# Kernel optimization log

Measured on AMD Instinct MI355X. Metric: run time of the kernel, lower is better.

The kernel has to match this reference:

```python
import jax, jax.numpy as jnp
import numpy as np

B, T, OBS, ACT, H, S = 512, 64, 1024, 32, 1024, 64


def setup_inputs() -> dict:
    key = jax.random.key(0)
    ks = jax.random.split(key, 16)
    w = lambda k, shape: 0.02 * jax.random.normal(k, shape, jnp.float32)
    return {
        "obs": jax.random.normal(ks[0], (B, T, OBS), jnp.float32),
        "action": jax.random.normal(ks[1], (B, T, ACT), jnp.float32),
        "eps": jax.random.normal(ks[2], (B, T, S), jnp.float32),
        # obs encoder: Linear(OBS->H) + ReLU
        "W_enc": w(ks[3], (H, OBS)), "b_enc": jnp.zeros((H,), jnp.float32),
        # GRUCell(stoch+action -> H), torch gate order: r, z, n
        "W_ih": w(ks[4], (3 * H, S + ACT)), "W_hh": w(ks[5], (3 * H, H)),
        "b_ih": jnp.zeros((3 * H,), jnp.float32), "b_hh": jnp.zeros((3 * H,), jnp.float32),
        # prior: Linear(H -> 2S); posterior: Linear(2H -> 2S)
        "W_prior": w(ks[6], (2 * S, H)), "b_prior": jnp.zeros((2 * S,), jnp.float32),
        "W_post": w(ks[7], (2 * S, 2 * H)), "b_post": jnp.zeros((2 * S,), jnp.float32),
        # decoder: Linear(H+S -> H) ReLU Linear(H -> OBS)
        "W_dec1": w(ks[8], (H, H + S)), "b_dec1": jnp.zeros((H,), jnp.float32),
        "W_dec2": w(ks[9], (OBS, H)), "b_dec2": jnp.zeros((OBS,), jnp.float32),
        # reward / done heads: Linear(H+S -> 1)
        "W_rew": w(ks[10], (1, H + S)), "b_rew": jnp.zeros((1,), jnp.float32),
        "W_done": w(ks[11], (1, H + S)), "b_done": jnp.zeros((1,), jnp.float32),
    }


def _stats(x):
    mean, raw_std = jnp.split(x, 2, axis=-1)
    return mean, jax.nn.softplus(raw_std) + 1e-4


def reference(obs, action, eps, W_enc, b_enc, W_ih, W_hh, b_ih, b_hh,
              W_prior, b_prior, W_post, b_post, W_dec1, b_dec1, W_dec2, b_dec2,
              W_rew, b_rew, W_done, b_done):
    batch = obs.shape[0]
    hid = W_hh.shape[1]
    sdim = eps.shape[-1]
    # obs encoder is per-step independent -> batch it over time up front
    emb_all = jax.nn.relu(jnp.einsum('bto,ho->bth', obs, W_enc) + b_enc)

    def step(carry, xs):
        deter, stoch = carry
        a_t, emb_t, eps_t = xs
        # torch GRUCell
        x = jnp.concatenate([stoch, a_t], axis=-1)
        gi = x @ W_ih.T + b_ih
        gh = deter @ W_hh.T + b_hh
        i_r, i_z, i_n = jnp.split(gi, 3, axis=-1)
        h_r, h_z, h_n = jnp.split(gh, 3, axis=-1)
        r = jax.nn.sigmoid(i_r + h_r)
        z = jax.nn.sigmoid(i_z + h_z)
        n = jnp.tanh(i_n + r * h_n)
        deter = (1.0 - z) * n + z * deter
        # prior / posterior stats
        p_mean, p_std = _stats(deter @ W_prior.T + b_prior)
        q_mean, q_std = _stats(jnp.concatenate([deter, emb_t], axis=-1) @ W_post.T + b_post)
        stoch = q_mean + eps_t * q_std  # reparam sample
        feat = jnp.concatenate([deter, stoch], axis=-1)
        pred = jax.nn.relu(feat @ W_dec1.T + b_dec1) @ W_dec2.T + b_dec2
        rew = feat @ W_rew.T + b_rew
        done = feat @ W_done.T + b_done
        kl = jnp.log(p_std / q_std) + (q_std ** 2 + (q_mean - p_mean) ** 2) / (2.0 * p_std ** 2) - 0.5
        return (deter, stoch), (pred, rew, done, kl.mean(axis=-1, keepdims=True))

    init = (jnp.zeros((batch, hid), obs.dtype), jnp.zeros((batch, sdim), obs.dtype))
    xs = (jnp.swapaxes(action, 0, 1), jnp.swapaxes(emb_all, 0, 1), jnp.swapaxes(eps, 0, 1))
    _, (preds, rews, dones, kls) = jax.lax.scan(step, init, xs)
    pred = jnp.swapaxes(preds, 0, 1)    # [B,T,OBS]
    reward = jnp.swapaxes(rews, 0, 1)   # [B,T,1]
    done = jnp.swapaxes(dones, 0, 1)    # [B,T,1]
    kl = kls.mean()
    return pred, reward, done, kl
```

## Files before the change

kernel.cpp:

```cpp
#include <hip/hip_runtime.h>
#include <stdint.h>

#define BB 512
#define TT 64
#define OBSD 1024
#define ACTD 32
#define HD 1024
#define SD 64
#define BT (BB*TT)
#define G3 (3*HD)
#define STRD ((long)TT*HD)

typedef unsigned int uint32;
typedef unsigned long long ull;
typedef unsigned short u16;
typedef __attribute__((ext_vector_type(8))) short bf16x8;
typedef __attribute__((ext_vector_type(4))) float f32x4;

__device__ __forceinline__ float bf2f(u16 v){ uint32_t u = ((uint32_t)v)<<16; return __builtin_bit_cast(float,u); }
__device__ __forceinline__ u16 f2bf(float f){ uint32_t u = __builtin_bit_cast(uint32_t,f); uint32_t r = (u + 0x7FFFu + ((u>>16)&1u))>>16; return (u16)r; }
__device__ __forceinline__ float sigm(float x){ return 1.f/(1.f+expf(-x)); }
#define MFMA __builtin_amdgcn_mfma_f32_16x16x32_bf16

__device__ __forceinline__ void gload16(const u16* g, u16* l){
  __builtin_amdgcn_global_load_lds(
      (const __attribute__((address_space(1))) u16*)g,
      (__attribute__((address_space(3))) u16*)l, 16, 0, 0);
}

__global__ void cvt_kernel(const float* __restrict__ in, u16* __restrict__ out, long n){
  long i = (long)blockIdx.x*blockDim.x + threadIdx.x;
  long st = (long)gridDim.x*blockDim.x;
  for (; i<n; i+=st) out[i] = f2bf(in[i]);
}

struct GemmP {
  const u16* a0; const u16* a1; const u16* a2;
  const u16* b0; const u16* b1; const u16* b2;
  long lda0, lda1, lda2, ldb0, ldb1, ldb2;
  int kc0, kc1, kc2, kcPerZ;
  float* cf; u16* cb;
  long ldc, ldcb, zstride;
  const float* bias0; const float* bias1;
  int relu;
};

template<int BM,int BN>
__global__ __launch_bounds__(256) void gemm_bf16(GemmP p){
  __shared__ __align__(16) u16 sAB[2][(BM+BN)*32];
  const int m0 = blockIdx.y*BM, n0 = blockIdx.x*BN;
  const int tid = threadIdx.x, lane = tid&63, wave = tid>>6;
  const int wm = (wave>>1)*(BM/2), wn = (wave&1)*(BN/2);
  constexpr int FM = BM/32, FN = BN/32;
  f32x4 acc[FM][FN] = {};
  const int cbeg = blockIdx.z*p.kcPerZ;
  int cend = cbeg + p.kcPerZ; if (cend > p.kc2) cend = p.kc2;
  const int kg = lane>>4, lr = lane&15;
  const int srow = lane>>2, scol = (lane&3)*8;

  auto STAGE = [&](int buf, int c){
    const u16* ap; const u16* bp; long lda, ldb; int kofs;
    if (c < p.kc0){ ap=p.a0; bp=p.b0; lda=p.lda0; ldb=p.ldb0; kofs=c*32; }
    else if (c < p.kc1){ ap=p.a1; bp=p.b1; lda=p.lda1; ldb=p.ldb1; kofs=(c-p.kc0)*32; }
    else { ap=p.a2; bp=p.b2; lda=p.lda2; ldb=p.ldb2; kofs=(c-p.kc1)*32; }
    u16* base = sAB[buf];
    #pragma unroll
    for (int it=0; it<BM/64; ++it){
      int row = it*64 + wave*16 + srow;
      gload16(ap + (long)(m0+row)*lda + kofs + scol,
              base + (it*64 + wave*16)*32);
    }
    #pragma unroll
    for (int it=0; it<BN/64; ++it){
      int row = it*64 + wave*16 + srow;
      gload16(bp + (long)(n0+row)*ldb + kofs + scol,
              base + BM*32 + (it*64 + wave*16)*32);
    }
  };

  STAGE(0, cbeg);
  for (int c=cbeg;c<cend;++c){
    const int cur = (c-cbeg)&1;
    asm volatile("s_waitcnt vmcnt(0)" ::: "memory");
    __syncthreads();
    if (c+1 < cend) STAGE(cur^1, c+1);
    const u16* sA = sAB[cur];
    const u16* sB = sAB[cur] + BM*32;
    bf16x8 af[FM], bfv[FN];
    #pragma unroll
    for (int i=0;i<FM;++i) af[i] = *(const bf16x8*)&sA[(wm+i*16+lr)*32 + kg*8];
    #pragma unroll
    for (int j=0;j<FN;++j) bfv[j] = *(const bf16x8*)&sB[(wn+j*16+lr)*32 + kg*8];
    #pragma unroll
    for (int i=0;i<FM;++i)
      #pragma unroll
      for (int j=0;j<FN;++j)
        acc[i][j] = MFMA(af[i], bfv[j], acc[i][j], 0,0,0);
    __syncthreads();
  }
  const bool partial = (gridDim.z > 1);
  float* cf = p.cf ? (p.cf + (partial ? (long)blockIdx.z*p.zstride : 0)) : nullptr;
  #pragma unroll
  for (int i=0;i<FM;++i){
    #pragma unroll
    for (int j=0;j<FN;++j){
      const int gr0 = m0 + wm + i*16 + kg*4;
      const int gc = n0 + wn + j*16 + lr;
      float bias = 0.f;
      if (!partial){
        if (p.bias0) bias += p.bias0[gc];
        if (p.bias1) bias += p.bias1[gc];
      }
      #pragma unroll
      for (int r=0;r<4;++r){
        float v = acc[i][j][r] + bias;
        if (p.relu) v = fmaxf(v, 0.f);
        const long row = gr0 + r;
        if (cf) cf[row*p.ldc + gc] = v;
        if (p.cb) p.cb[row*p.ldcb + gc] = f2bf(v);
      }
    }
  }
}

struct ScanArgs {
  const u16* act; const u16* Wih; const u16* Whh;
  const float* b_ih; const float* b_hh;
  const u16* Wpos; const float* qemb; const float* eps;
  u16* det; u16* sto; float* qm; float* qs;
  uint32* slots;
};

__device__ __forceinline__ void gsync_g(uint32* slots, int m, int n, uint32 val){
  asm volatile("s_waitcnt vmcnt(0)" ::: "memory");
  __syncthreads();
  if (threadIdx.x == 0)
    __hip_atomic_store(&slots[m*64 + n], val, __ATOMIC_RELAXED, __HIP_MEMORY_SCOPE_AGENT);
  if (threadIdx.x < 32){
    while (__hip_atomic_load(&slots[m*64 + threadIdx.x], __ATOMIC_RELAXED,
                             __HIP_MEMORY_SCOPE_AGENT) < val)
      __builtin_amdgcn_s_sleep(2);
  }
  __syncthreads();
}

#define SA2 152

__global__ __launch_bounds__(256, 1) void scan_kernel(ScanArgs A){
  __shared__ __align__(16) u16 lds[(64+96)*SA2];
  u16* sA = lds; u16* sB = lds + 64*SA2;
  float* pf = (float*)lds;
  const int bid = blockIdx.x;
  const int tid = threadIdx.x, lane = tid&63, wave = tid>>6;
  const int lr = lane&15, kg = lane>>4;
  const int n = bid&31, m = bid>>5;
  const int m0 = m*64, h0 = n*32;
  const int wrow = (wave&1)*32, wcol = (wave>>1)*16;

  const int srow = tid>>4;
  const int scu  = (tid&15)*8;

  long whhb[6], wihb[6];
  #pragma unroll
  for (int i=0;i<6;++i){
    int br = srow + i*16;
    int gate = br>>5, hr = br&31;
    whhb[i] = (long)(gate*HD + h0 + hr)*HD + scu;
    wihb[i] = (long)(gate*HD + h0 + hr)*96 + scu;
  }

  const int h4 = h0 + wcol + kg*4;
  float bir[4], bhr[4], biz[4], bhz[4], bin[4], bhn[4];
  #pragma unroll
  for (int r=0;r<4;++r){
    bir[r]=A.b_ih[h4+r];      bhr[r]=A.b_hh[h4+r];
    biz[r]=A.b_ih[HD+h4+r];   bhz[r]=A.b_hh[HD+h4+r];
    bin[r]=A.b_ih[2*HD+h4+r]; bhn[r]=A.b_hh[2*HD+h4+r];
  }

  const int pj = n & 3, prt = n >> 2;

  float dreg[2][4] = {{0.f,0.f,0.f,0.f},{0.f,0.f,0.f,0.f}};
  const bf16x8 zerov = {};

  bf16x8 pa[4], pb[6];
  auto loadgt = [&](int tt, int g){
    if (g < 8){
      if (tt > 0){
        const u16* s = A.det + (long)(tt-1)*HD + g*128 + scu;
        #pragma unroll
        for (int j=0;j<4;++j) pa[j] = *(const bf16x8*)(s + (long)(m0+srow+16*j)*STRD);
      } else { pa[0]=zerov; pa[1]=zerov; pa[2]=zerov; pa[3]=zerov; }
      #pragma unroll
      for (int i=0;i<6;++i) pb[i] = *(const bf16x8*)(A.Whh + whhb[i] + g*128);
    } else {
      if (scu < 64){
        if (tt > 0){
          #pragma unroll
          for (int j=0;j<4;++j)
            pa[j] = *(const bf16x8*)(A.sto + (long)(m0+srow+16*j)*((long)TT*SD) + (long)(tt-1)*SD + scu);
        } else { pa[0]=zerov; pa[1]=zerov; pa[2]=zerov; pa[3]=zerov; }
      } else if (scu < 96){
        #pragma unroll
        for (int j=0;j<4;++j)
          pa[j] = *(const bf16x8*)(A.act + (long)(m0+srow+16*j)*((long)TT*ACTD) + (long)tt*ACTD + (scu-64));
      } else { pa[0]=zerov; pa[1]=zerov; pa[2]=zerov; pa[3]=zerov; }
      #pragma unroll
      for (int i=0;i<6;++i) pb[i] = (scu < 96) ? *(const bf16x8*)(A.Wih + wihb[i]) : zerov;
    }
  };

  loadgt(0, 0);
  for (int t=0; t<TT; ++t){
    f32x4 aR[2]={}, aZ[2]={}, aNd[2]={}, aNx[2]={};
    for (int g=0; g<9; ++g){
      __syncthreads();
      #pragma unroll
      for (int j=0;j<4;++j) *(bf16x8*)&sA[(srow+16*j)*SA2 + scu] = pa[j];
      #pragma unroll
      for (int i=0;i<6;++i) *(bf16x8*)&sB[(srow+16*i)*SA2 + scu] = pb[i];
      if (g < 8) loadgt(t, g+1);
      __syncthreads();
      #pragma unroll
      for (int k=0;k<4;++k){
        bf16x8 a0v = *(const bf16x8*)&sA[(wrow+lr)*SA2 + k*32 + kg*8];
        bf16x8 a1v = *(const bf16x8*)&sA[(wrow+16+lr)*SA2 + k*32 + kg*8];
        bf16x8 b0 = *(const bf16x8*)&sB[(wcol+lr)*SA2 + k*32 + kg*8];
        bf16x8 b1 = *(const bf16x8*)&sB[(32+wcol+lr)*SA2 + k*32 + kg*8];
        bf16x8 b2 = *(const bf16x8*)&sB[(64+wcol+lr)*SA2 + k*32 + kg*8];
        aR[0] = MFMA(b0,a0v,aR[0],0,0,0); aR[1] = MFMA(b0,a1v,aR[1],0,0,0);
        aZ[0] = MFMA(b1,a0v,aZ[0],0,0,0); aZ[1] = MFMA(b1,a1v,aZ[1],0,0,0);
        if (g<8){ aNd[0] = MFMA(b2,a0v,aNd[0],0,0,0); aNd[1] = MFMA(b2,a1v,aNd[1],0,0,0); }
        else    { aNx[0] = MFMA(b2,a0v,aNx[0],0,0,0); aNx[1] = MFMA(b2,a1v,aNx[1],0,0,0); }
      }
    }
    #pragma unroll
    for (int rf=0;rf<2;++rf){
      const long brow = m0 + wrow + rf*16 + lr;
      u16 pk[4];
      #pragma unroll
      for (int r=0;r<4;++r){
        float rr = sigm(aR[rf][r]+bir[r]+bhr[r]);
        float z  = sigm(aZ[rf][r]+biz[r]+bhz[r]);
        float nn = tanhf(aNx[rf][r]+bin[r] + rr*(aNd[rf][r]+bhn[r]));
        float d = (1.f - z)*nn + z*dreg[rf][r];
        dreg[rf][r] = d;
        pk[r] = f2bf(d);
      }
      ull pv; __builtin_memcpy(&pv, pk, 8);
      __hip_atomic_store((ull*)(A.det + brow*STRD + (long)t*HD + h4), pv,
                         __ATOMIC_RELAXED, __HIP_MEMORY_SCOPE_AGENT);
    }
    gsync_g(A.slots, m, n, (uint32)(2*t+1));
    {
      f32x4 accM = {}, accS = {};
      const int k0 = wave*256;
      const u16* arow = A.det + (long)(m0 + prt*8 + (lr&7))*STRD + (long)t*HD + k0 + kg*8;
      const u16* bm = A.Wpos + (long)(pj*16 + lr)*(2*HD) + k0 + kg*8;
      const u16* bs = A.Wpos + (long)(64 + pj*16 + lr)*(2*HD) + k0 + kg*8;
      #pragma unroll
      for (int kk=0; kk<8; ++kk){
        bf16x8 af = *(const bf16x8*)(arow + kk*32);
        accM = MFMA(af, *(const bf16x8*)(bm + kk*32), accM, 0,0,0);
        accS = MFMA(af, *(const bf16x8*)(bs + kk*32), accS, 0,0,0);
      }
      #pragma unroll
      for (int r=0;r<4;++r){
        int rowt = kg*4 + r;
        pf[wave*512 + rowt*16 + lr]       = accM[r];
        pf[wave*512 + 256 + rowt*16 + lr] = accS[r];
      }
      __syncthreads();
      if (tid < 64){
        const int row = tid>>3;
        const int s2 = (tid&7)*2;
        const long grow = m0 + prt*8 + row;
        const float* qe = A.qemb + grow*((long)TT*128) + (long)t*128;
        const float* ep = A.eps  + grow*((long)TT*SD) + (long)t*SD;
        u16 spk[2];
        #pragma unroll
        for (int i=0;i<2;++i){
          int sl = s2 + i, sg = pj*16 + sl;
          float mean = pf[row*16+sl] + pf[512+row*16+sl] + pf[1024+row*16+sl] + pf[1536+row*16+sl];
          float rsv  = pf[256+row*16+sl] + pf[768+row*16+sl] + pf[1280+row*16+sl] + pf[1792+row*16+sl];
          mean += qe[sg];
          rsv  += qe[64+sg];
          float sp = fmaxf(rsv,0.f) + log1pf(expf(-fabsf(rsv)));
          float qs_ = sp + 1e-4f;
          float st = mean + ep[sg]*qs_;
          A.qm[grow*((long)TT*SD) + (long)t*SD + sg] = mean;
          A.qs[grow*((long)TT*SD) + (long)t*SD + sg] = qs_;
          spk[i] = f2bf(st);
        }
        uint32 pv; __builtin_memcpy(&pv, spk, 4);
        __hip_atomic_store((uint32*)(A.sto + grow*((long)TT*SD) + (long)t*SD + pj*16 + s2), pv,
                           __ATOMIC_RELAXED, __HIP_MEMORY_SCOPE_AGENT);
      }
      __syncthreads();
    }
    if (t+1 < TT) loadgt(t+1, 0);
    gsync_g(A.slots, m, n, (uint32)(2*t+2));
  }
}

__global__ __launch_bounds__(256) void gru_step(
    const u16* __restrict__ sto_prev, long ssto,
    const u16* __restrict__ act_t,
    const u16* __restrict__ det_prev, long sdet,
    const u16* __restrict__ Wih, const u16* __restrict__ Whh,
    const float* __restrict__ b_ih, const float* __restrict__ b_hh,
    float* __restrict__ deterF, u16* __restrict__ det_bf_t){
  constexpr int SA = 40;
  __shared__ u16 sA[32*SA];
  __shared__ u16 sB[96*SA];
  const int id = blockIdx.x;
  const int n = (id&7) + ((id>>7)<<3);
  const int m = (id>>3)&15;
  const int m0 = m*32, h0 = n*32;
  const int tid = threadIdx.x, lane = tid&63, wave = tid>>6;
  const int wm = wave>>1, wn = wave&1;
  const int lr = lane&15, kg = lane>>4;

  f32x4 aR = {}, aZ = {}, aNd = {}, aNx = {};

  auto aAddr = [&](int c, int row, int sc)->const u16*{
    if (c < 32) return det_prev + (long)(m0+row)*sdet + c*32 + sc;
    if (c < 34) return sto_prev + (long)(m0+row)*ssto + (c-32)*32 + sc;
    return act_t + (long)(m0+row)*((long)TT*ACTD) + sc;
  };
  auto bAddr = [&](int c, int l)->const u16*{
    int row = l>>2, sc = (l&3)*8;
    int g = row>>5, hr = row&31;
    if (c < 32) return Whh + (long)(g*1024 + h0 + hr)*HD + c*32 + sc;
    return Wih + (long)(g*1024 + h0 + hr)*(SD+ACTD) + (c-32)*32 + sc;
  };

  bf16x8 rA, rB0, rB1;
  auto loadc = [&](int c){
    rB0 = *(const bf16x8*)bAddr(c, tid);
    if (tid < 128){
      rA  = *(const bf16x8*)aAddr(c, tid>>2, (tid&3)*8);
      rB1 = *(const bf16x8*)bAddr(c, 256+tid);
    }
  };

  loadc(0);
  for (int c=0; c<35; ++c){
    *(bf16x8*)&sB[(tid>>2)*SA + (tid&3)*8] = rB0;
    if (tid < 128){
      *(bf16x8*)&sA[(tid>>2)*SA + (tid&3)*8] = rA;
      int l = 256+tid;
      *(bf16x8*)&sB[(l>>2)*SA + (l&3)*8] = rB1;
    }
    if (c < 34) loadc(c+1);
    __syncthreads();
    bf16x8 af = *(const bf16x8*)&sA[(wm*16+lr)*SA + kg*8];
    bf16x8 b0 = *(const bf16x8*)&sB[(     wn*16+lr)*SA + kg*8];
    bf16x8 b1 = *(const bf16x8*)&sB[(32 + wn*16+lr)*SA + kg*8];
    bf16x8 b2 = *(const bf16x8*)&sB[(64 + wn*16+lr)*SA + kg*8];
    aR = MFMA(af,b0,aR,0,0,0);
    aZ = MFMA(af,b1,aZ,0,0,0);
    if (c < 32) aNd = MFMA(af,b2,aNd,0,0,0);
    else        aNx = MFMA(af,b2,aNx,0,0,0);
    __syncthreads();
  }

  const int col = h0 + wn*16 + lr;
  const float bir = b_ih[col],      bhr = b_hh[col];
  const float biz = b_ih[col+HD],   bhz = b_hh[col+HD];
  const float bin = b_ih[col+2*HD], bhn = b_hh[col+2*HD];
  #pragma unroll
  for (int reg=0; reg<4; ++reg){
    const int row = m0 + wm*16 + kg*4 + reg;
    float r = sigm(aR[reg] + bir + bhr);
    float z = sigm(aZ[reg] + biz + bhz);
    float nn = tanhf(aNx[reg] + bin + r*(aNd[reg] + bhn));
    const long fidx = (long)row*HD + col;
    float d = (1.f - z)*nn + z*deterF[fidx];
    deterF[fidx] = d;
    det_bf_t[(long)row*STRD + col] = f2bf(d);
  }
}

__global__ __launch_bounds__(256) void post_step(
    const u16* __restrict__ det_t,
    const u16* __restrict__ Wpos,
    const float* __restrict__ qemb_t,
    const float* __restrict__ eps_t,
    float* __restrict__ qm_t, float* __restrict__ qs_t, u16* __restrict__ sto_out){
  constexpr int SA = 40;
  __shared__ u16 sA4[4*16*SA];
  __shared__ u16 sB4[4*128*SA];
  const int m0 = blockIdx.x*16;
  const int tid = threadIdx.x, lane = tid&63, w = tid>>6;
  const int lr = lane&15, kg = lane>>4;

  f32x4 acc[8] = {};
  bf16x8 rA, rB[8];
  auto loadIter = [&](int i){
    #pragma unroll
    for (int rnd=0; rnd<8; ++rnd){
      int l = rnd*256 + tid;
      int q = l>>9, row = (l>>2)&127, sc = (l&3)*8;
      rB[rnd] = *(const bf16x8*)(Wpos + (long)row*(2*HD) + (q*8+i)*32 + sc);
    }
    { int q = tid>>6, row = (tid>>2)&15, sc = (tid&3)*8;
      rA = *(const bf16x8*)(det_t + (long)(m0+row)*STRD + (q*8+i)*32 + sc); }
  };

  loadIter(0);
  for (int i=0; i<8; ++i){
    #pragma unroll
    for (int rnd=0; rnd<8; ++rnd){
      int l = rnd*256 + tid;
      int q = l>>9, row = (l>>2)&127, sc = (l&3)*8;
      *(bf16x8*)&sB4[q*128*SA + row*SA + sc] = rB[rnd];
    }
    { int q = tid>>6, row = (tid>>2)&15, sc = (tid&3)*8;
      *(bf16x8*)&sA4[q*16*SA + row*SA + sc] = rA; }
    if (i < 7) loadIter(i+1);
    __syncthreads();
    bf16x8 af = *(const bf16x8*)&sA4[w*16*SA + lr*SA + kg*8];
    #pragma unroll
    for (int j=0; j<8; ++j){
      bf16x8 bf = *(const bf16x8*)&sB4[w*128*SA + (j*16+lr)*SA + kg*8];
      acc[j] = MFMA(af, bf, acc[j], 0,0,0);
    }
    __syncthreads();
  }

  float* pf = (float*)sB4;
  #pragma unroll
  for (int j=0; j<8; ++j)
    #pragma unroll
    for (int reg=0; reg<4; ++reg)
      pf[w*2048 + (kg*4+reg)*128 + j*16+lr] = acc[j][reg];
  __syncthreads();

  #pragma unroll
  for (int i=0; i<4; ++i){
    int p = tid + i*256;
    int row = p>>6, s = p&63;
    int b = m0 + row;
    float mval = pf[row*128+s]      + pf[2048+row*128+s]      + pf[4096+row*128+s]      + pf[6144+row*128+s];
    float rsv  = pf[row*128+64+s]   + pf[2048+row*128+64+s]   + pf[4096+row*128+64+s]   + pf[6144+row*128+64+s];
    mval += qemb_t[(long)b*((long)TT*128) + s];
    rsv  += qemb_t[(long)b*((long)TT*128) + 64 + s];
    float sp = fmaxf(rsv,0.f) + log1pf(expf(-fabsf(rsv)));
    float qsv = sp + 1e-4f;
    float e = eps_t[(long)b*((long)TT*SD) + s];
    float st = mval + e*qsv;
    qm_t[(long)b*((long)TT*SD) + s] = mval;
    qs_t[(long)b*((long)TT*SD) + s] = qsv;
    sto_out[(long)b*((long)TT*SD) + s] = f2bf(st);
  }
}

__global__ void kl_kernel(const float* __restrict__ pbuf, const float* __restrict__ qm,
                          const float* __restrict__ qs, float* __restrict__ klrows){
  int m = blockIdx.x*4 + (threadIdx.x>>6);
  int s = threadIdx.x & 63;
  float pm   = pbuf[(long)m*128 + s];
  float praw = pbuf[(long)m*128 + 64 + s];
  float ps = fmaxf(praw,0.f) + log1pf(expf(-fabsf(praw))) + 1e-4f;
  float qmv = qm[(long)m*64+s], qsv = qs[(long)m*64+s];
  float d = qmv - pm;
  float kl = logf(ps/qsv) + (qsv*qsv + d*d)/(2.f*ps*ps) - 0.5f;
  #pragma unroll
  for (int off=32; off; off>>=1) kl += __shfl_xor(kl, off);
  if (s==0) klrows[m] = kl*(1.f/64.f);
}

__global__ void kl_reduce(const float* __restrict__ klrows, float* __restrict__ out){
  __shared__ float sm[256];
  float a = 0.f;
  for (int i=threadIdx.x; i<BT; i+=256) a += klrows[i];
  sm[threadIdx.x]=a; __syncthreads();
  for (int off=128; off; off>>=1){ if ((int)threadIdx.x<off) sm[threadIdx.x]+=sm[threadIdx.x+off]; __syncthreads(); }
  if (threadIdx.x==0) out[0] = sm[0] / (float)BT;
}

__global__ void rewdone_kernel(const u16* __restrict__ det, const u16* __restrict__ sto,
    const float* __restrict__ Wr, const float* __restrict__ br,
    const float* __restrict__ Wd, const float* __restrict__ bd,
    float* __restrict__ orew, float* __restrict__ odone){
  int m = blockIdx.x*4 + (threadIdx.x>>6);
  int lane = threadIdx.x & 63;
  float ar=0.f, ad=0.f;
  for (int k=lane; k<HD+SD; k+=64){
    float f = (k<HD) ? bf2f(det[(long)m*HD+k]) : bf2f(sto[(long)m*SD + (k-HD)]);
    ar = fmaf(f, Wr[k], ar); ad = fmaf(f, Wd[k], ad);
  }
  #pragma unroll
  for (int off=32; off; off>>=1){ ar += __shfl_xor(ar, off); ad += __shfl_xor(ad, off); }
  if (lane==0){ orew[m]=ar+br[0]; odone[m]=ad+bd[0]; }
}

static char* carve(char*& base, size_t bytes){
  char* p = base; base += (bytes + 255) & ~(size_t)255; return p;
}

extern "C" void kernel_launch(void* const* d_in, const int* in_sizes, int n_in,
                              void* d_out, int out_size, void* d_ws, size_t ws_size,
                              hipStream_t stream) {
  const float* obs    = (const float*)d_in[0];
  const float* action = (const float*)d_in[1];
  const float* eps    = (const float*)d_in[2];
  const float* W_enc  = (const float*)d_in[3];
  const float* b_enc  = (const float*)d_in[4];
  const float* W_ih   = (const float*)d_in[5];
  const float* W_hh   = (const float*)d_in[6];
  const float* b_ih   = (const float*)d_in[7];
  const float* b_hh   = (const float*)d_in[8];
  const float* W_prior= (const float*)d_in[9];
  const float* b_prior= (const float*)d_in[10];
  const float* W_post = (const float*)d_in[11];
  const float* b_post = (const float*)d_in[12];
  const float* W_dec1 = (const float*)d_in[13];
  const float* b_dec1 = (const float*)d_in[14];
  const float* W_dec2 = (const float*)d_in[15];
  const float* b_dec2 = (const float*)d_in[16];
  const float* W_rew  = (const float*)d_in[17];
  const float* b_rew  = (const float*)d_in[18];
  const float* W_done = (const float*)d_in[19];
  const float* b_done = (const float*)d_in[20];

  char* w = (char*)d_ws;
  u16* obs_bf  = (u16*)carve(w, (size_t)BT*OBSD*2);
  u16* emb_bf  = (u16*)carve(w, (size_t)BT*HD*2);
  u16* det_bf  = (u16*)carve(w, (size_t)BT*HD*2);
  u16* sto_bf  = (u16*)carve(w, (size_t)BT*SD*2);
  u16* act_bf  = (u16*)carve(w, (size_t)BT*ACTD*2);
  u16* Wenc_bf = (u16*)carve(w, (size_t)HD*OBSD*2);
  u16* Wih_bf  = (u16*)carve(w, (size_t)G3*(SD+ACTD)*2);
  u16* Whh_bf  = (u16*)carve(w, (size_t)G3*HD*2);
  u16* Wpri_bf = (u16*)carve(w, (size_t)2*SD*HD*2);
  u16* Wpos_bf = (u16*)carve(w, (size_t)2*SD*2*HD*2);
  u16* Wd1_bf  = (u16*)carve(w, (size_t)HD*(HD+SD)*2);
  u16* Wd2_bf  = (u16*)carve(w, (size_t)OBSD*HD*2);
  u16* zero_bf = (u16*)carve(w, 4096);
  float* deterF = (float*)carve(w, (size_t)BB*HD*4);
  float* qemb   = (float*)carve(w, (size_t)BT*128*4);
  float* qm_all = (float*)carve(w, (size_t)BT*SD*4);
  float* qs_all = (float*)carve(w, (size_t)BT*SD*4);
  float* p_buf  = (float*)carve(w, (size_t)BT*2*SD*4);
  float* klrows = (float*)carve(w, (size_t)BT*4);
  uint32* syncb = (uint32*)carve(w, 8192);
  u16* hid_bf = obs_bf;

  if ((size_t)(w - (char*)d_ws) > ws_size){
    hipMemsetAsync(d_out, 0xFF, 4, stream);
    return;
  }

  auto cvt = [&](const float* in, u16* out, long n){
    cvt_kernel<<<dim3(2048), dim3(256), 0, stream>>>(in, out, n);
  };
  cvt(obs, obs_bf, (long)BT*OBSD);
  cvt(action, act_bf, (long)BT*ACTD);
  cvt(W_enc, Wenc_bf, (long)HD*OBSD);
  cvt(W_ih, Wih_bf, (long)G3*(SD+ACTD));
  cvt(W_hh, Whh_bf, (long)G3*HD);
  cvt(W_prior, Wpri_bf, (long)2*SD*HD);
  cvt(W_post, Wpos_bf, (long)2*SD*2*HD);
  cvt(W_dec1, Wd1_bf, (long)HD*(HD+SD));
  cvt(W_dec2, Wd2_bf, (long)OBSD*HD);
  hipMemsetAsync(zero_bf, 0, 4096, stream);
  hipMemsetAsync(deterF, 0, (size_t)BB*HD*4, stream);
  hipMemsetAsync(syncb, 0, 8192, stream);

  {
    GemmP q{};
    q.a0 = obs_bf;  q.lda0 = OBSD;
    q.b0 = Wenc_bf; q.ldb0 = OBSD;
    q.kc0=q.kc1=q.kc2=32; q.kcPerZ=32;
    q.cb = emb_bf; q.ldcb = HD;
    q.bias0 = b_enc; q.relu = 1;
    gemm_bf16<128,128><<<dim3(HD/128, BT/128, 1), 256, 0, stream>>>(q);
  }
  {
    GemmP q{};
    q.a0 = emb_bf;       q.lda0 = HD;
    q.b0 = Wpos_bf + HD; q.ldb0 = 2*HD;
    q.kc0=q.kc1=q.kc2=32; q.kcPerZ=32;
    q.cf = qemb; q.ldc = 128;
    q.bias0 = b_post;
    gemm_bf16<64,64><<<dim3(128/64, BT/64, 1), 256, 0, stream>>>(q);
  }

  {
    ScanArgs sa;
    sa.act = act_bf; sa.Wih = Wih_bf; sa.Whh = Whh_bf;
    sa.b_ih = b_ih; sa.b_hh = b_hh;
    sa.Wpos = Wpos_bf; sa.qemb = qemb; sa.eps = eps;
    sa.det = det_bf; sa.sto = sto_bf; sa.qm = qm_all; sa.qs = qs_all;
    sa.slots = syncb;
    void* kargs[] = { (void*)&sa };
    hipError_t cerr = hipLaunchCooperativeKernel((const void*)scan_kernel,
        dim3(256), dim3(256), kargs, 0, stream);
    if (cerr != hipSuccess){
      for (int t=0; t<TT; ++t){
        const u16* sto_p = (t==0) ? zero_bf : (sto_bf + (long)(t-1)*SD);
        long ssto        = (t==0) ? 0 : (long)TT*SD;
        const u16* det_p = (t==0) ? zero_bf : (det_bf + (long)(t-1)*HD);
        long sdet        = (t==0) ? 0 : STRD;
        gru_step<<<dim3(512), 256, 0, stream>>>(sto_p, ssto, act_bf + (long)t*ACTD,
            det_p, sdet, Wih_bf, Whh_bf, b_ih, b_hh, deterF, det_bf + (long)t*HD);
        post_step<<<dim3(32), 256, 0, stream>>>(det_bf + (long)t*HD, Wpos_bf,
            qemb + (long)t*128, eps + (long)t*SD,
            qm_all + (long)t*SD, qs_all + (long)t*SD, sto_bf + (long)t*SD);
      }
    }
  }

  {
    GemmP q{};
    q.a0 = det_bf;  q.lda0 = HD;
    q.b0 = Wpri_bf; q.ldb0 = HD;
    q.kc0=q.kc1=q.kc2=32; q.kcPerZ=32;
    q.cf = p_buf; q.ldc = 2*SD;
    q.bias0 = b_prior;
    gemm_bf16<64,64><<<dim3(2*SD/64, BT/64, 1), 256, 0, stream>>>(q);
  }
  kl_kernel<<<dim3(BT/4), 256, 0, stream>>>(p_buf, qm_all, qs_all, klrows);
  {
    GemmP q{};
    q.a0 = det_bf; q.lda0 = HD;
    q.a1 = sto_bf; q.lda1 = SD;
    q.b0 = Wd1_bf;      q.ldb0 = HD+SD;
    q.b1 = Wd1_bf + HD; q.ldb1 = HD+SD;
    q.kc0=32; q.kc1=34; q.kc2=34; q.kcPerZ=34;
    q.cb = hid_bf; q.ldcb = HD;
    q.bias0 = b_dec1; q.relu = 1;
    gemm_bf16<128,128><<<dim3(HD/128, BT/128, 1), 256, 0, stream>>>(q);
  }
  {
    GemmP q{};
    q.a0 = hid_bf; q.lda0 = HD;
    q.b0 = Wd2_bf; q.ldb0 = HD;
    q.kc0=q.kc1=q.kc2=32; q.kcPerZ=32;
    q.cf = (float*)d_out; q.ldc = OBSD;
    q.bias0 = b_dec2;
    gemm_bf16<128,128><<<dim3(OBSD/128, BT/128, 1), 256, 0, stream>>>(q);
  }
  rewdone_kernel<<<dim3(BT/4), 256, 0, stream>>>(det_bf, sto_bf, W_rew, b_rew, W_done, b_done,
      (float*)d_out + (long)BT*OBSD, (float*)d_out + (long)BT*OBSD + BT);
  kl_reduce<<<dim3(1), 256, 0, stream>>>(klrows, (float*)d_out + (long)BT*OBSD + 2*BT);
}
```

Before: 1.672 ms.

## Feed GRU MFMAs directly from global memory, removing LDS staging and barriers

The recurrent scan kernel no longer stages deter/stoch/action and W_ih/W_hh tiles through shared memory. Each wave now loads its own MFMA operand fragments straight from global memory, 32-wide K chunks at a time, and prefetches only the next chunk in registers. The goal is to remove the two __syncthreads per K group and the LDS write/read round trip. In exchange, waves that share rows now load the same data redundantly, and only one small chunk is in flight, so each step may be limited by global-load latency. A zero buffer pointer is added so the t=0 case can reuse the same load path with stride zero.

```diff
diff --git a/kernel.cpp b/kernel.cpp
--- a/kernel.cpp
+++ b/kernel.cpp
@@ -128,7 +128,7 @@
   const float* b_ih; const float* b_hh;
   const u16* Wpos; const float* qemb; const float* eps;
   u16* det; u16* sto; float* qm; float* qs;
-  uint32* slots;
+  uint32* slots; const u16* zeroB;
 };
 
 __device__ __forceinline__ void gsync_g(uint32* slots, int m, int n, uint32 val){
@@ -144,30 +144,14 @@
   __syncthreads();
 }
 
-#define SA2 152
-
 __global__ __launch_bounds__(256, 1) void scan_kernel(ScanArgs A){
-  __shared__ __align__(16) u16 lds[(64+96)*SA2];
-  u16* sA = lds; u16* sB = lds + 64*SA2;
-  float* pf = (float*)lds;
+  __shared__ __align__(16) float pf[2048];
   const int bid = blockIdx.x;
   const int tid = threadIdx.x, lane = tid&63, wave = tid>>6;
   const int lr = lane&15, kg = lane>>4;
   const int n = bid&31, m = bid>>5;
   const int m0 = m*64, h0 = n*32;
   const int wrow = (wave&1)*32, wcol = (wave>>1)*16;
-
-  const int srow = tid>>4;
-  const int scu  = (tid&15)*8;
-
-  long whhb[6], wihb[6];
-  #pragma unroll
-  for (int i=0;i<6;++i){
-    int br = srow + i*16;
-    int gate = br>>5, hr = br&31;
-    whhb[i] = (long)(gate*HD + h0 + hr)*HD + scu;
-    wihb[i] = (long)(gate*HD + h0 + hr)*96 + scu;
-  }
 
   const int h4 = h0 + wcol + kg*4;
   float bir[4], bhr[4], biz[4], bhz[4], bin[4], bhn[4];
@@ -181,59 +165,61 @@
   const int pj = n & 3, prt = n >> 2;
 
   float dreg[2][4] = {{0.f,0.f,0.f,0.f},{0.f,0.f,0.f,0.f}};
-  const bf16x8 zerov = {};
-
-  bf16x8 pa[4], pb[6];
-  auto loadgt = [&](int tt, int g){
-    if (g < 8){
-      if (tt > 0){
-        const u16* s = A.det + (long)(tt-1)*HD + g*128 + scu;
-        #pragma unroll
-        for (int j=0;j<4;++j) pa[j] = *(const bf16x8*)(s + (long)(m0+srow+16*j)*STRD);
-      } else { pa[0]=zerov; pa[1]=zerov; pa[2]=zerov; pa[3]=zerov; }
-      #pragma unroll
-      for (int i=0;i<6;++i) pb[i] = *(const bf16x8*)(A.Whh + whhb[i] + g*128);
+
+  const long ar0 = (long)(m0 + wrow + lr);
+  const long ar1 = (long)(m0 + wrow + 16 + lr);
+  const long bw  = (long)(h0 + wcol + lr);
+
+  bf16x8 ca0, ca1, cb0, cb1, cb2;
+  auto issue_c = [&](const u16* dB, long dS, const u16* stB, long sS, int tt, int c,
+                     bf16x8& a0, bf16x8& a1, bf16x8& b0, bf16x8& b1, bf16x8& b2){
+    if (c < 32){
+      const u16* s = dB + c*32 + kg*8;
+      a0 = *(const bf16x8*)(s + ar0*dS);
+      a1 = *(const bf16x8*)(s + ar1*dS);
+      const u16* wb = A.Whh + bw*HD + c*32 + kg*8;
+      b0 = *(const bf16x8*)wb;
+      b1 = *(const bf16x8*)(wb + (long)HD*HD);
+      b2 = *(const bf16x8*)(wb + (long)2*HD*HD);
+    } else if (c < 34){
+      const u16* s = stB + (c-32)*32 + kg*8;
+      a0 = *(const bf16x8*)(s + ar0*sS);
+      a1 = *(const bf16x8*)(s + ar1*sS);
+      const u16* wb = A.Wih + bw*96 + (c-32)*32 + kg*8;
+      b0 = *(const bf16x8*)wb;
+      b1 = *(const bf16x8*)(wb + (long)HD*96);
+      b2 = *(const bf16x8*)(wb + (long)2*HD*96);
     } else {
-      if (scu < 64){
-        if (tt > 0){
-          #pragma unroll
-          for (int j=0;j<4;++j)
-            pa[j] = *(const bf16x8*)(A.sto + (long)(m0+srow+16*j)*((long)TT*SD) + (long)(tt-1)*SD + scu);
-        } else { pa[0]=zerov; pa[1]=zerov; pa[2]=zerov; pa[3]=zerov; }
-      } else if (scu < 96){
-        #pragma unroll
-        for (int j=0;j<4;++j)
-          pa[j] = *(const bf16x8*)(A.act + (long)(m0+srow+16*j)*((long)TT*ACTD) + (long)tt*ACTD + (scu-64));
-      } else { pa[0]=zerov; pa[1]=zerov; pa[2]=zerov; pa[3]=zerov; }
-      #pragma unroll
-      for (int i=0;i<6;++i) pb[i] = (scu < 96) ? *(const bf16x8*)(A.Wih + wihb[i]) : zerov;
+      const u16* s = A.act + (long)tt*ACTD + kg*8;
+      a0 = *(const bf16x8*)(s + ar0*((long)TT*ACTD));
+      a1 = *(const bf16x8*)(s + ar1*((long)TT*ACTD));
+      const u16* wb = A.Wih + bw*96 + 64 + kg*8;
+      b0 = *(const bf16x8*)wb;
+      b1 = *(const bf16x8*)(wb + (long)HD*96);
+      b2 = *(const bf16x8*)(wb + (long)2*HD*96);
     }
   };
 
-  loadgt(0, 0);
+  issue_c(A.zeroB, 0, A.zeroB, 0, 0, 0, ca0,ca1,cb0,cb1,cb2);
+
   for (int t=0; t<TT; ++t){
+    const u16* dB  = (t>0) ? (A.det + (long)(t-1)*HD) : A.zeroB;
+    const long dS  = (t>0) ? STRD : 0;
+    const u16* stB = (t>0) ? (A.sto + (long)(t-1)*SD) : A.zeroB;
+    const long sS  = (t>0) ? (long)TT*SD : 0;
+
     f32x4 aR[2]={}, aZ[2]={}, aNd[2]={}, aNx[2]={};
-    for (int g=0; g<9; ++g){
-      __syncthreads();
-      #pragma unroll
-      for (int j=0;j<4;++j) *(bf16x8*)&sA[(srow+16*j)*SA2 + scu] = pa[j];
-      #pragma unroll
-      for (int i=0;i<6;++i) *(bf16x8*)&sB[(srow+16*i)*SA2 + scu] = pb[i];
-      if (g < 8) loadgt(t, g+1);
-      __syncthreads();
-      #pragma unroll
-      for (int k=0;k<4;++k){
-        bf16x8 a0v = *(const bf16x8*)&sA[(wrow+lr)*SA2 + k*32 + kg*8];
-        bf16x8 a1v = *(const bf16x8*)&sA[(wrow+16+lr)*SA2 + k*32 + kg*8];
-        bf16x8 b0 = *(const bf16x8*)&sB[(wcol+lr)*SA2 + k*32 + kg*8];
-        bf16x8 b1 = *(const bf16x8*)&sB[(32+wcol+lr)*SA2 + k*32 + kg*8];
-        bf16x8 b2 = *(const bf16x8*)&sB[(64+wcol+lr)*SA2 + k*32 + kg*8];
-        aR[0] = MFMA(b0,a0v,aR[0],0,0,0); aR[1] = MFMA(b0,a1v,aR[1],0,0,0);
-        aZ[0] = MFMA(b1,a0v,aZ[0],0,0,0); aZ[1] = MFMA(b1,a1v,aZ[1],0,0,0);
-        if (g<8){ aNd[0] = MFMA(b2,a0v,aNd[0],0,0,0); aNd[1] = MFMA(b2,a1v,aNd[1],0,0,0); }
-        else    { aNx[0] = MFMA(b2,a0v,aNx[0],0,0,0); aNx[1] = MFMA(b2,a1v,aNx[1],0,0,0); }
-      }
-    }
+    #pragma unroll
+    for (int c=0; c<35; ++c){
+      bf16x8 na0, na1, nb0, nb1, nb2;
+      if (c < 34) issue_c(dB, dS, stB, sS, t, c+1, na0,na1,nb0,nb1,nb2);
+      aR[0] = MFMA(cb0,ca0,aR[0],0,0,0); aR[1] = MFMA(cb0,ca1,aR[1],0,0,0);
+      aZ[0] = MFMA(cb1,ca0,aZ[0],0,0,0); aZ[1] = MFMA(cb1,ca1,aZ[1],0,0,0);
+      if (c < 32){ aNd[0] = MFMA(cb2,ca0,aNd[0],0,0,0); aNd[1] = MFMA(cb2,ca1,aNd[1],0,0,0); }
+      else       { aNx[0] = MFMA(cb2,ca0,aNx[0],0,0,0); aNx[1] = MFMA(cb2,ca1,aNx[1],0,0,0); }
+      if (c < 34){ ca0=na0; ca1=na1; cb0=nb0; cb1=nb1; cb2=nb2; }
+    }
+
     #pragma unroll
     for (int rf=0;rf<2;++rf){
       const long brow = m0 + wrow + rf*16 + lr;
@@ -252,6 +238,7 @@
                          __ATOMIC_RELAXED, __HIP_MEMORY_SCOPE_AGENT);
     }
     gsync_g(A.slots, m, n, (uint32)(2*t+1));
+
     {
       f32x4 accM = {}, accS = {};
       const int k0 = wave*256;
@@ -298,7 +285,8 @@
       }
       __syncthreads();
     }
-    if (t+1 < TT) loadgt(t+1, 0);
+    if (t+1 < TT)
+      issue_c(A.det + (long)t*HD, STRD, A.zeroB, 0, t+1, 0, ca0,ca1,cb0,cb1,cb2);
     gsync_g(A.slots, m, n, (uint32)(2*t+2));
   }
 }
@@ -594,7 +582,7 @@
     sa.b_ih = b_ih; sa.b_hh = b_hh;
     sa.Wpos = Wpos_bf; sa.qemb = qemb; sa.eps = eps;
     sa.det = det_bf; sa.sto = sto_bf; sa.qm = qm_all; sa.qs = qs_all;
-    sa.slots = syncb;
+    sa.slots = syncb; sa.zeroB = zero_bf;
     void* kargs[] = { (void*)&sa };
     hipError_t cerr = hipLaunchCooperativeKernel((const void*)scan_kernel,
         dim3(256), dim3(256), kargs, 0, stream);
```

Result: slower. 2.733 ms (+63.4%).

## Add 32-row scan kernel running 512 cooperative blocks, two per CU

Applied to the files above, without the earlier changes.

Adds a new cooperative recurrent-scan kernel that splits the batch into 32-row tiles instead of 64-row tiles. This launches 512 blocks, two resident per CU, which halves per-block GRU and posterior work on each time step and doubles the number of blocks working on the sequential scan. The posterior projection is repartitioned so each block handles 4 rows by 16 stochastic dims. The old 64-row kernel and the per-step launch path stay as fallbacks. The cost is more blocks taking part in every grid barrier, and each block gets less register and LDS budget.

```diff
diff --git a/kernel.cpp b/kernel.cpp
--- a/kernel.cpp
+++ b/kernel.cpp
@@ -128,7 +128,7 @@
   const float* b_ih; const float* b_hh;
   const u16* Wpos; const float* qemb; const float* eps;
   u16* det; u16* sto; float* qm; float* qs;
-  uint32* slots;
+  uint32* slots; const u16* zeroB;
 };
 
 __device__ __forceinline__ void gsync_g(uint32* slots, int m, int n, uint32 val){
@@ -144,9 +144,159 @@
   __syncthreads();
 }
 
+#define SA3 76
+
+__global__ __launch_bounds__(256, 2) void scan_kernel32(ScanArgs A){
+  __shared__ __align__(16) u16 lds[(32+96)*SA3];
+  u16* sA = lds; u16* sB = lds + 32*SA3;
+  float* pf = (float*)lds;
+  const int bid = blockIdx.x;
+  const int tid = threadIdx.x, lane = tid&63, wave = tid>>6;
+  const int lr = lane&15, kg = lane>>4;
+  const int n = bid&31, m = bid>>5;
+  const int m0 = m*32, h0 = n*32;
+  const int wrow = (wave&1)*16, wcol = (wave>>1)*16;
+
+  const int srow8 = tid>>3;
+  const int scu8  = (tid&7)*8;
+
+  const int h4 = h0 + wcol + kg*4;
+  float bir[4], bhr[4], biz[4], bhz[4], bin[4], bhn[4];
+  #pragma unroll
+  for (int r=0;r<4;++r){
+    bir[r]=A.b_ih[h4+r];      bhr[r]=A.b_hh[h4+r];
+    biz[r]=A.b_ih[HD+h4+r];   bhz[r]=A.b_hh[HD+h4+r];
+    bin[r]=A.b_ih[2*HD+h4+r]; bhn[r]=A.b_hh[2*HD+h4+r];
+  }
+
+  const int pj = n & 3, prt = n >> 2;
+
+  float dreg[4] = {0.f,0.f,0.f,0.f};
+  const bf16x8 zerov = {};
+
+  bf16x8 pa, pb[3];
+  auto loadgt = [&](int tt, int g){
+    if (g < 16){
+      if (tt > 0)
+        pa = *(const bf16x8*)(A.det + (long)(m0+srow8)*STRD + (long)(tt-1)*HD + g*64 + scu8);
+      else pa = zerov;
+      #pragma unroll
+      for (int i=0;i<3;++i)
+        pb[i] = *(const bf16x8*)(A.Whh + (long)(i*HD + h0 + srow8)*HD + g*64 + scu8);
+    } else if (g == 16){
+      if (tt > 0)
+        pa = *(const bf16x8*)(A.sto + (long)(m0+srow8)*((long)TT*SD) + (long)(tt-1)*SD + scu8);
+      else pa = zerov;
+      #pragma unroll
+      for (int i=0;i<3;++i)
+        pb[i] = *(const bf16x8*)(A.Wih + (long)(i*HD + h0 + srow8)*96 + scu8);
+    } else {
+      if (scu8 < 32){
+        pa = *(const bf16x8*)(A.act + (long)(m0+srow8)*((long)TT*ACTD) + (long)tt*ACTD + scu8);
+        #pragma unroll
+        for (int i=0;i<3;++i)
+          pb[i] = *(const bf16x8*)(A.Wih + (long)(i*HD + h0 + srow8)*96 + 64 + scu8);
+      } else {
+        pa = zerov;
+        pb[0]=zerov; pb[1]=zerov; pb[2]=zerov;
+      }
+    }
+  };
+
+  loadgt(0, 0);
+  for (int t=0; t<TT; ++t){
+    f32x4 aR={}, aZ={}, aNd={}, aNx={};
+    for (int g=0; g<18; ++g){
+      __syncthreads();
+      *(bf16x8*)&sA[srow8*SA3 + scu8] = pa;
+      #pragma unroll
+      for (int i=0;i<3;++i) *(bf16x8*)&sB[(srow8 + i*32)*SA3 + scu8] = pb[i];
+      if (g < 17) loadgt(t, g+1);
+      __syncthreads();
+      #pragma unroll
+      for (int k=0;k<2;++k){
+        bf16x8 av = *(const bf16x8*)&sA[(wrow+lr)*SA3 + k*32 + kg*8];
+        bf16x8 b0 = *(const bf16x8*)&sB[(wcol+lr)*SA3 + k*32 + kg*8];
+        bf16x8 b1 = *(const bf16x8*)&sB[(32+wcol+lr)*SA3 + k*32 + kg*8];
+        bf16x8 b2 = *(const bf16x8*)&sB[(64+wcol+lr)*SA3 + k*32 + kg*8];
+        aR = MFMA(b0,av,aR,0,0,0);
+        aZ = MFMA(b1,av,aZ,0,0,0);
+        if (g<16) aNd = MFMA(b2,av,aNd,0,0,0);
+        else      aNx = MFMA(b2,av,aNx,0,0,0);
+      }
+    }
+    {
+      const long brow = m0 + wrow + lr;
+      u16 pk[4];
+      #pragma unroll
+      for (int r=0;r<4;++r){
+        float rr = sigm(aR[r]+bir[r]+bhr[r]);
+        float z  = sigm(aZ[r]+biz[r]+bhz[r]);
+        float nn = tanhf(aNx[r]+bin[r] + rr*(aNd[r]+bhn[r]));
+        float d = (1.f - z)*nn + z*dreg[r];
+        dreg[r] = d;
+        pk[r] = f2bf(d);
+      }
+      ull pv; __builtin_memcpy(&pv, pk, 8);
+      __hip_atomic_store((ull*)(A.det + brow*STRD + (long)t*HD + h4), pv,
+                         __ATOMIC_RELAXED, __HIP_MEMORY_SCOPE_AGENT);
+    }
+    gsync_g(A.slots, m, n, (uint32)(2*t+1));
+
+    {
+      f32x4 accM = {}, accS = {};
+      const int k0 = wave*256;
+      const u16* arow = A.det + (long)(m0 + prt*4 + (lr&3))*STRD + (long)t*HD + k0 + kg*8;
+      const u16* bm = A.Wpos + (long)(pj*16 + lr)*(2*HD) + k0 + kg*8;
+      const u16* bs = A.Wpos + (long)(64 + pj*16 + lr)*(2*HD) + k0 + kg*8;
+      #pragma unroll
+      for (int kk=0; kk<8; ++kk){
+        bf16x8 af = *(const bf16x8*)(arow + kk*32);
+        accM = MFMA(af, *(const bf16x8*)(bm + kk*32), accM, 0,0,0);
+        accS = MFMA(af, *(const bf16x8*)(bs + kk*32), accS, 0,0,0);
+      }
+      #pragma unroll
+      for (int r=0;r<4;++r){
+        int rowt = kg*4 + r;
+        pf[wave*512 + rowt*16 + lr]       = accM[r];
+        pf[wave*512 + 256 + rowt*16 + lr] = accS[r];
+      }
+      __syncthreads();
+      if (tid < 32){
+        const int row = tid>>3;
+        const int s2 = (tid&7)*2;
+        const long grow = m0 + prt*4 + row;
+        const float* qe = A.qemb + grow*((long)TT*128) + (long)t*128;
+        const float* ep = A.eps  + grow*((long)TT*SD) + (long)t*SD;
+        u16 spk[2];
+        #pragma unroll
+        for (int i=0;i<2;++i){
+          int sl = s2 + i, sg = pj*16 + sl;
+          float mean = pf[row*16+sl] + pf[512+row*16+sl] + pf[1024+row*16+sl] + pf[1536+row*16+sl];
+          float rsv  = pf[256+row*16+sl] + pf[768+row*16+sl] + pf[1280+row*16+sl] + pf[1792+row*16+sl];
+          mean += qe[sg];
+          rsv  += qe[64+sg];
+          float sp = fmaxf(rsv,0.f) + log1pf(expf(-fabsf(rsv)));
+          float qs_ = sp + 1e-4f;
+          float st = mean + ep[sg]*qs_;
+          A.qm[grow*((long)TT*SD) + (long)t*SD + sg] = mean;
+          A.qs[grow*((long)TT*SD) + (long)t*SD + sg] = qs_;
+          spk[i] = f2bf(st);
+        }
+        uint32 pv; __builtin_memcpy(&pv, spk, 4);
+        __hip_atomic_store((uint32*)(A.sto + grow*((long)TT*SD) + (long)t*SD + pj*16 + s2), pv,
+                           __ATOMIC_RELAXED, __HIP_MEMORY_SCOPE_AGENT);
+      }
+      __syncthreads();
+    }
+    if (t+1 < TT) loadgt(t+1, 0);
+    gsync_g(A.slots, m, n, (uint32)(2*t+2));
+  }
+}
+
 #define SA2 152
 
-__global__ __launch_bounds__(256, 1) void scan_kernel(ScanArgs A){
+__global__ __launch_bounds__(256, 1) void scan_kernel64(ScanArgs A){
   __shared__ __align__(16) u16 lds[(64+96)*SA2];
   u16* sA = lds; u16* sB = lds + 64*SA2;
   float* pf = (float*)lds;
@@ -594,21 +744,25 @@
     sa.b_ih = b_ih; sa.b_hh = b_hh;
     sa.Wpos = Wpos_bf; sa.qemb = qemb; sa.eps = eps;
     sa.det = det_bf; sa.sto = sto_bf; sa.qm = qm_all; sa.qs = qs_all;
-    sa.slots = syncb;
+    sa.slots = syncb; sa.zeroB = zero_bf;
     void* kargs[] = { (void*)&sa };
-    hipError_t cerr = hipLaunchCooperativeKernel((const void*)scan_kernel,
-        dim3(256), dim3(256), kargs, 0, stream);
-    if (cerr != hipSuccess){
-      for (int t=0; t<TT; ++t){
-        const u16* sto_p = (t==0) ? zero_bf : (sto_bf + (long)(t-1)*SD);
-        long ssto        = (t==0) ? 0 : (long)TT*SD;
-        const u16* det_p = (t==0) ? zero_bf : (det_bf + (long)(t-1)*HD);
-        long sdet        = (t==0) ? 0 : STRD;
-        gru_step<<<dim3(512), 256, 0, stream>>>(sto_p, ssto, act_bf + (long)t*ACTD,
-            det_p, sdet, Wih_bf, Whh_bf, b_ih, b_hh, deterF, det_bf + (long)t*HD);
-        post_step<<<dim3(32), 256, 0, stream>>>(det_bf + (long)t*HD, Wpos_bf,
-            qemb + (long)t*128, eps + (long)t*SD,
-            qm_all + (long)t*SD, qs_all + (long)t*SD, sto_bf + (long)t*SD);
+    hipError_t e1 = hipLaunchCooperativeKernel((const void*)scan_kernel32,
+        dim3(512), dim3(256), kargs, 0, stream);
+    if (e1 != hipSuccess){
+      hipError_t e2 = hipLaunchCooperativeKernel((const void*)scan_kernel64,
+          dim3(256), dim3(256), kargs, 0, stream);
+      if (e2 != hipSuccess){
+        for (int t=0; t<TT; ++t){
+          const u16* sto_p = (t==0) ? zero_bf : (sto_bf + (long)(t-1)*SD);
+          long ssto        = (t==0) ? 0 : (long)TT*SD;
+          const u16* det_p = (t==0) ? zero_bf : (det_bf + (long)(t-1)*HD);
+          long sdet        = (t==0) ? 0 : STRD;
+          gru_step<<<dim3(512), 256, 0, stream>>>(sto_p, ssto, act_bf + (long)t*ACTD,
+              det_p, sdet, Wih_bf, Whh_bf, b_ih, b_hh, deterF, det_bf + (long)t*HD);
+          post_step<<<dim3(32), 256, 0, stream>>>(det_bf + (long)t*HD, Wpos_bf,
+              qemb + (long)t*128, eps + (long)t*SD,
+              qm_all + (long)t*SD, qs_all + (long)t*SD, sto_bf + (long)t*SD);
+        }
       }
     }
   }
```

Measured after the change: 3.549 ms. 112% more time.
